# Optimization experiments

Measured on AMD Instinct MI355X. Metric: run time of the kernel, lower is better.

The kernel has to match this reference:

```python
import jax, jax.numpy as jnp
import numpy as np

C_Z = 128
C_H = 128
L = 512
EPS = 1e-5


def _layer_norm(x, w, b):
    mu = jnp.mean(x, axis=-1, keepdims=True)
    var = jnp.mean(jnp.square(x - mu), axis=-1, keepdims=True)
    return (x - mu) * jax.lax.rsqrt(var + EPS) * w + b


def setup_inputs() -> dict:
    key = jax.random.key(0)
    ks = jax.random.split(key, 10)
    s_z = 1.0 / np.sqrt(C_Z)
    s_h = 1.0 / np.sqrt(C_H)
    return {
        "z": jax.random.normal(ks[0], (L, L, C_Z), dtype=jnp.float32),
        "pair_mask": jax.random.randint(ks[1], (L, L), 0, 2, dtype=jnp.int32),
        "ln_in_w": jnp.ones((C_Z,), jnp.float32),
        "ln_in_b": jnp.zeros((C_Z,), jnp.float32),
        "ln_out_w": jnp.ones((C_H,), jnp.float32),
        "ln_out_b": jnp.zeros((C_H,), jnp.float32),
        # weights stored [in, out] so forward is x @ W
        "W_proj_a": jax.random.uniform(ks[2], (C_Z, C_H), jnp.float32, -s_z, s_z),
        "W_gate_a": jax.random.uniform(ks[3], (C_Z, C_H), jnp.float32, -s_z, s_z),
        "W_proj_b": jax.random.uniform(ks[4], (C_Z, C_H), jnp.float32, -s_z, s_z),
        "W_gate_b": jax.random.uniform(ks[5], (C_Z, C_H), jnp.float32, -s_z, s_z),
        "W_gate_out": jax.random.uniform(ks[6], (C_Z, C_Z), jnp.float32, -s_z, s_z),
        "W_proj_out": jax.random.uniform(ks[7], (C_H, C_Z), jnp.float32, -s_h, s_h),
    }


def reference(z, pair_mask, ln_in_w, ln_in_b, ln_out_w, ln_out_b,
              W_proj_a, W_gate_a, W_proj_b, W_gate_b, W_gate_out, W_proj_out):
    mask = pair_mask.astype(z.dtype)[..., None]  # [L, L, 1]
    z_ln = _layer_norm(z, ln_in_w, ln_in_b)      # [L, L, c_z]
    a = jax.nn.sigmoid(z_ln @ W_gate_a) * (z_ln @ W_proj_a) * mask  # [L, L, c_h]
    b = jax.nn.sigmoid(z_ln @ W_gate_b) * (z_ln @ W_proj_b) * mask  # [L, L, c_h]
    m = jnp.einsum('ikc,jkc->ijc', a, b)         # channel-batched matmul
    m_ln = _layer_norm(m, ln_out_w, ln_out_b)
    g = jax.nn.sigmoid(z_ln @ W_gate_out)        # [L, L, c_z]
    dz = g * (m_ln @ W_proj_out)
    return dz * mask
```

## Files before the change

### kernel.cpp

```cpp
#include <hip/hip_runtime.h>
#include <stdint.h>

#define LDIM 512
#define LLTOT 262144
#define EPSV 1e-5f

typedef short bf16x8 __attribute__((ext_vector_type(8)));
typedef float f32x4 __attribute__((ext_vector_type(4)));
typedef __attribute__((address_space(1))) unsigned as1_u32;
typedef __attribute__((address_space(3))) unsigned as3_u32;

__device__ __forceinline__ void stage16(const void* g, void* l) {
  __builtin_amdgcn_global_load_lds((as1_u32*)g, (as3_u32*)l, 16, 0, 0);
}

__device__ __forceinline__ unsigned short f2bf(float f) {
  union { float f; unsigned u; } v; v.f = f;
  unsigned r = v.u + 0x7FFFu + ((v.u >> 16) & 1u);
  return (unsigned short)(r >> 16);
}
__device__ __forceinline__ float bf2f(unsigned short h) {
  union { unsigned u; float f; } v; v.u = ((unsigned)h) << 16;
  return v.f;
}
__device__ __forceinline__ unsigned cvtpk(float lo, float hi) {
  unsigned r;
  asm("v_cvt_pk_bf16_f32 %0, %1, %2" : "=v"(r) : "v"(lo), "v"(hi));
  return r;
}
__device__ __forceinline__ float sigm(float x) { return 1.0f / (1.0f + __expf(-x)); }


__global__ void k_prep(const float* __restrict__ Wpa, const float* __restrict__ Wga,
                       const float* __restrict__ Wpb, const float* __restrict__ Wgb,
                       const float* __restrict__ Wgo, const float* __restrict__ Wpo,
                       unsigned short* __restrict__ Wt) {
  int t = blockIdx.x * blockDim.x + threadIdx.x;
  int mat = t >> 14;
  int rem = t & 16383;
  int o = rem >> 7;
  int c = rem & 127;
  const float* src;
  switch (mat) {
    case 0: src = Wga; break;
    case 1: src = Wpa; break;
    case 2: src = Wgb; break;
    case 3: src = Wpb; break;
    case 4: src = Wgo; break;
    default: src = Wpo; break;
  }
  Wt[mat * 16384 + o * 128 + c] = f2bf(src[c * 128 + o]);
}

__global__ __launch_bounds__(256, 4) void k_proj(const float* __restrict__ z,
                                                 const float* __restrict__ lnw,
                                                 const float* __restrict__ lnb,
                                                 const unsigned short* __restrict__ Wt,
                                                 const int* __restrict__ maskp,
                                                 unsigned short* __restrict__ a_f,
                                                 unsigned short* __restrict__ b_f,
                                                 unsigned short* __restrict__ gout) {
  __shared__ __align__(16) unsigned char zbuf[128 * 272];
  __shared__ float maskf[128];
  const int t = threadIdx.x;
  const int bid = blockIdx.x;
  const long r0 = (long)bid * 128;
  const int w = t >> 6, lane = t & 63;
  const int mn = lane & 15, q4 = lane >> 4;
  const int k0 = (bid & 3) * 128;
  const long ibase = (long)(bid >> 2) * 131072;

  if (t < 128) maskf[t] = (float)maskp[r0 + t];

  {
    const int sub = lane >> 4, c16 = lane & 15;
    const float4 lw0 = ((const float4*)lnw)[c16 * 2];
    const float4 lw1 = ((const float4*)lnw)[c16 * 2 + 1];
    const float4 lb0 = ((const float4*)lnb)[c16 * 2];
    const float4 lb1 = ((const float4*)lnb)[c16 * 2 + 1];
#pragma unroll 2
    for (int rr = 0; rr < 8; ++rr) {
      const int row = w * 32 + rr * 4 + sub;
      const float4* zr = (const float4*)(z + (r0 + row) * 128);
      float4 v0 = zr[c16 * 2], v1 = zr[c16 * 2 + 1];
      float s = ((v0.x + v0.y) + (v0.z + v0.w)) + ((v1.x + v1.y) + (v1.z + v1.w));
      float q = v0.x * v0.x + v0.y * v0.y + v0.z * v0.z + v0.w * v0.w +
                v1.x * v1.x + v1.y * v1.y + v1.z * v1.z + v1.w * v1.w;
#pragma unroll
      for (int off = 8; off; off >>= 1) { s += __shfl_xor(s, off); q += __shfl_xor(q, off); }
      float mu = s * (1.0f / 128.0f);
      float rs = rsqrtf(q * (1.0f / 128.0f) - mu * mu + EPSV);
      uint4 o;
      o.x = cvtpk((v0.x - mu) * rs * lw0.x + lb0.x, (v0.y - mu) * rs * lw0.y + lb0.y);
      o.y = cvtpk((v0.z - mu) * rs * lw0.z + lb0.z, (v0.w - mu) * rs * lw0.w + lb0.w);
      o.z = cvtpk((v1.x - mu) * rs * lw1.x + lb1.x, (v1.y - mu) * rs * lw1.y + lb1.y);
      o.w = cvtpk((v1.z - mu) * rs * lw1.z + lb1.z, (v1.w - mu) * rs * lw1.w + lb1.w);
      *(uint4*)(&zbuf[row * 272 + c16 * 16]) = o;
    }
  }
  __syncthreads();

#pragma unroll 1
  for (int p = 0; p < 2; ++p) {
    const unsigned short* Wg = Wt + (p * 2) * 16384;
    const unsigned short* Wp = Wt + (p * 2 + 1) * 16384;
    unsigned short* dst = p ? b_f : a_f;
    bf16x8 wg[2][4], wp[2][4];
#pragma unroll
    for (int ntl = 0; ntl < 2; ++ntl)
#pragma unroll
      for (int kk = 0; kk < 4; ++kk) {
        const int o = (w * 2 + ntl) * 16 + mn;
        wg[ntl][kk] = *(const bf16x8*)(Wg + o * 128 + kk * 32 + q4 * 8);
        wp[ntl][kk] = *(const bf16x8*)(Wp + o * 128 + kk * 32 + q4 * 8);
      }
#pragma unroll 1
    for (int rg = 0; rg < 8; ++rg) {
      bf16x8 afr[4];
#pragma unroll
      for (int kk = 0; kk < 4; ++kk)
        afr[kk] = *(const bf16x8*)(&zbuf[(rg * 16 + mn) * 272 + kk * 64 + q4 * 16]);
      f32x4 aG[2] = {{0.f,0.f,0.f,0.f},{0.f,0.f,0.f,0.f}};
      f32x4 aP[2] = {{0.f,0.f,0.f,0.f},{0.f,0.f,0.f,0.f}};
#pragma unroll
      for (int kk = 0; kk < 4; ++kk)
#pragma unroll
        for (int ntl = 0; ntl < 2; ++ntl) {
          aG[ntl] = __builtin_amdgcn_mfma_f32_16x16x32_bf16(afr[kk], wg[ntl][kk], aG[ntl], 0, 0, 0);
          aP[ntl] = __builtin_amdgcn_mfma_f32_16x16x32_bf16(afr[kk], wp[ntl][kk], aP[ntl], 0, 0, 0);
        }
      const int rowb = rg * 16 + q4 * 4;
      const int kpos = k0 + rowb;
      char* dst0 = (char*)dst + ibase + (kpos >> 5) * 8192 + (kpos & 31) * 2;
#pragma unroll
      for (int ntl = 0; ntl < 2; ++ntl) {
        const int c = (w * 2 + ntl) * 16 + mn;
        float e0 = sigm(aG[ntl][0]) * aP[ntl][0] * maskf[rowb + 0];
        float e1 = sigm(aG[ntl][1]) * aP[ntl][1] * maskf[rowb + 1];
        float e2 = sigm(aG[ntl][2]) * aP[ntl][2] * maskf[rowb + 2];
        float e3 = sigm(aG[ntl][3]) * aP[ntl][3] * maskf[rowb + 3];
        uint2 pk;
        pk.x = cvtpk(e0, e1);
        pk.y = cvtpk(e2, e3);
        *(uint2*)(dst0 + c * 64) = pk;
      }
    }
  }

  {
    const unsigned short* Wgp = Wt + 4 * 16384;
    bf16x8 wg[2][4];
#pragma unroll
    for (int ntl = 0; ntl < 2; ++ntl)
#pragma unroll
      for (int kk = 0; kk < 4; ++kk)
        wg[ntl][kk] = *(const bf16x8*)(Wgp + ((w * 2 + ntl) * 16 + mn) * 128 + kk * 32 + q4 * 8);
#pragma unroll 1
    for (int rg = 0; rg < 8; ++rg) {
      bf16x8 afr[4];
#pragma unroll
      for (int kk = 0; kk < 4; ++kk)
        afr[kk] = *(const bf16x8*)(&zbuf[(rg * 16 + mn) * 272 + kk * 64 + q4 * 16]);
      f32x4 aG[2] = {{0.f,0.f,0.f,0.f},{0.f,0.f,0.f,0.f}};
#pragma unroll
      for (int kk = 0; kk < 4; ++kk)
#pragma unroll
        for (int ntl = 0; ntl < 2; ++ntl)
          aG[ntl] = __builtin_amdgcn_mfma_f32_16x16x32_bf16(afr[kk], wg[ntl][kk], aG[ntl], 0, 0, 0);
      const int rowb = rg * 16 + q4 * 4;
#pragma unroll
      for (int ntl = 0; ntl < 2; ++ntl) {
        const int c = (w * 2 + ntl) * 16 + mn;
        unsigned u01 = cvtpk(sigm(aG[ntl][0]), sigm(aG[ntl][1]));
        unsigned u23 = cvtpk(sigm(aG[ntl][2]), sigm(aG[ntl][3]));
        gout[(r0 + rowb + 0) * 128 + c] = (unsigned short)u01;
        gout[(r0 + rowb + 1) * 128 + c] = (unsigned short)(u01 >> 16);
        gout[(r0 + rowb + 2) * 128 + c] = (unsigned short)u23;
        gout[(r0 + rowb + 3) * 128 + c] = (unsigned short)(u23 >> 16);
      }
    }
  }
}

__global__ __launch_bounds__(256, 3) void k_einsum(const unsigned short* __restrict__ af_g,
                                                   const unsigned short* __restrict__ bf_g,
                                                   unsigned short* __restrict__ m_t) {
  __shared__ __align__(16) unsigned char shm[49152];
  const int t = threadIdx.x;
  const int w = t >> 6, lane = t & 63;
  const int bid = blockIdx.x;
  const int xcd = bid & 7;
  const int j = bid >> 3;
  const int ch = xcd * 16 + (j >> 4);
  const int tile = j & 15;
  const int ti = tile >> 2, tj = tile & 3;
  const int wr = w >> 1, wc = w & 1;
  const int mn = lane & 15, q4 = lane >> 4;
  const int loff = (mn * 4 + q4) * 16;

  const long lanepart = (long)(lane >> 2) * 131072 + (lane & 3) * 16 + ch * 64;

  const char* gsrc[4];
#pragma unroll
  for (int u = 0; u < 4; ++u) {
    const int f = w * 4 + u;
    gsrc[u] = (f < 8)
        ? (const char*)af_g + (long)(ti * 8 + f) * 16 * 131072 + lanepart
        : (const char*)bf_g + (long)(tj * 8 + (f - 8)) * 16 * 131072 + lanepart;
  }

  f32x4 acc[4][4];
#pragma unroll
  for (int i = 0; i < 4; ++i)
#pragma unroll
    for (int jj = 0; jj < 4; ++jj) acc[i][jj] = (f32x4){0.f, 0.f, 0.f, 0.f};

#define STAGE(q, k32)                                                          \
  {                                                                            \
    _Pragma("unroll")                                                          \
    for (int u = 0; u < 4; ++u)                                                \
      stage16(gsrc[u] + (long)(k32) * 8192,                                    \
              &shm[(q) * 16384 + (w * 4 + u) * 1024]);                         \
  }

  STAGE(0, 0)
  STAGE(1, 1)
#pragma unroll 1
  for (int k32 = 0; k32 < 16; ++k32) {
    if (k32 < 15) {
      asm volatile("s_waitcnt vmcnt(4)\n\ts_barrier" ::: "memory");
    } else {
      asm volatile("s_waitcnt vmcnt(0)\n\ts_barrier" ::: "memory");
    }
    if (k32 + 2 < 16) STAGE((k32 + 2) % 3, k32 + 2)
    const int cb = (k32 % 3) * 16384;
    bf16x8 afr[4], bfr[4];
#pragma unroll
    for (int mt = 0; mt < 4; ++mt)
      afr[mt] = *(const bf16x8*)(&shm[cb + (wr * 4 + mt) * 1024 + loff]);
#pragma unroll
    for (int nt = 0; nt < 4; ++nt)
      bfr[nt] = *(const bf16x8*)(&shm[cb + 8192 + (wc * 4 + nt) * 1024 + loff]);
#pragma unroll
    for (int mt = 0; mt < 4; ++mt)
#pragma unroll
      for (int nt = 0; nt < 4; ++nt)
        acc[mt][nt] = __builtin_amdgcn_mfma_f32_16x16x32_bf16(
            afr[mt], bfr[nt], acc[mt][nt], 0, 0, 0);
  }
#undef STAGE
  __syncthreads();

  unsigned char* eb = shm + w * 9216;
#pragma unroll
  for (int mt = 0; mt < 4; ++mt)
#pragma unroll
    for (int nt = 0; nt < 4; ++nt) {
      const int rlb = mt * 16 + q4 * 4;
      const int cl = nt * 16 + mn;
      unsigned u01 = cvtpk(acc[mt][nt][0], acc[mt][nt][1]);
      unsigned u23 = cvtpk(acc[mt][nt][2], acc[mt][nt][3]);
      *(unsigned short*)(&eb[(rlb + 0) * 144 + cl * 2]) = (unsigned short)u01;
      *(unsigned short*)(&eb[(rlb + 1) * 144 + cl * 2]) = (unsigned short)(u01 >> 16);
      *(unsigned short*)(&eb[(rlb + 2) * 144 + cl * 2]) = (unsigned short)u23;
      *(unsigned short*)(&eb[(rlb + 3) * 144 + cl * 2]) = (unsigned short)(u23 >> 16);
    }
  char* Mg = (char*)m_t + (long)ch * 524288 +
             (long)(ti * 128 + wr * 64) * 1024 + (tj * 128 + wc * 64) * 2;
#pragma unroll
  for (int it = 0; it < 8; ++it) {
    int rl = it * 8 + (lane >> 3), cc = lane & 7;
    *(int4*)(Mg + (long)rl * 1024 + cc * 16) = *(const int4*)(&eb[rl * 144 + cc * 16]);
  }
}

__global__ __launch_bounds__(256, 3) void k_out(const unsigned short* __restrict__ m_t,
                                                const unsigned short* __restrict__ gbuf,
                                                const unsigned short* __restrict__ Wt,
                                                const int* __restrict__ maskp,
                                                const float* __restrict__ lnw,
                                                const float* __restrict__ lnb,
                                                float* __restrict__ out) {
  __shared__ unsigned char mln[64 * 272];
  __shared__ float obuf[64 * 132];
  __shared__ float lw[128], lb[128], mk[64];
  const int t = threadIdx.x;
  const long r0 = (long)blockIdx.x * 64;

#pragma unroll
  for (int it = 0; it < 4; ++it) {
    int chunk = it * 256 + t;
    int c = chunk >> 3, cc = chunk & 7;
    int4 rv = *(const int4*)((const char*)m_t + (long)c * 524288 + r0 * 2 + cc * 16);
    const unsigned short* rp = (const unsigned short*)&rv;
#pragma unroll
    for (int e = 0; e < 8; ++e) {
      int er = (e + cc) & 7;
      *(unsigned short*)(&mln[(cc * 8 + er) * 272 + c * 2]) = rp[er];
    }
  }
  if (t < 128) { lw[t] = lnw[t]; lb[t] = lnb[t]; }
  if (t < 64) mk[t] = (float)maskp[r0 + t];
  __syncthreads();

  {
    int row = t >> 2, part = t & 3;
    float xv[32];
    float s = 0.f, q = 0.f;
#pragma unroll
    for (int jj = 0; jj < 16; ++jj) {
      unsigned u = *(const unsigned*)(&mln[row * 272 + part * 64 + jj * 4]);
      float x0 = bf2f((unsigned short)(u & 0xffff));
      float x1 = bf2f((unsigned short)(u >> 16));
      xv[2 * jj] = x0; xv[2 * jj + 1] = x1;
      s += x0 + x1; q += x0 * x0 + x1 * x1;
    }
    s += __shfl_xor(s, 1); q += __shfl_xor(q, 1);
    s += __shfl_xor(s, 2); q += __shfl_xor(q, 2);
    float mu = s * (1.f / 128.f);
    float var = q * (1.f / 128.f) - mu * mu;
    float rs = rsqrtf(var + EPSV);
#pragma unroll
    for (int jj = 0; jj < 16; ++jj) {
      int c = part * 32 + 2 * jj;
      unsigned pk = cvtpk((xv[2 * jj] - mu) * rs * lw[c] + lb[c],
                          (xv[2 * jj + 1] - mu) * rs * lw[c + 1] + lb[c + 1]);
      *(unsigned*)(&mln[row * 272 + c * 2]) = pk;
    }
  }
  __syncthreads();

  const int w = t >> 6, lane = t & 63;
  const int mn = lane & 15, q4 = lane >> 4;
  bf16x8 afr[4];
#pragma unroll
  for (int kk = 0; kk < 4; ++kk)
    afr[kk] = *(const bf16x8*)(&mln[(w * 16 + mn) * 272 + kk * 64 + q4 * 16]);
  const unsigned short* Wp = Wt + 5 * 16384;
#pragma unroll 1
  for (int nt = 0; nt < 8; ++nt) {
    f32x4 acc = {0.f, 0.f, 0.f, 0.f};
#pragma unroll
    for (int kk = 0; kk < 4; ++kk) {
      bf16x8 bfr = *(const bf16x8*)(Wp + (nt * 16 + mn) * 128 + kk * 32 + q4 * 8);
      acc = __builtin_amdgcn_mfma_f32_16x16x32_bf16(afr[kk], bfr, acc, 0, 0, 0);
    }
    const int cl = nt * 16 + mn;
#pragma unroll
    for (int r = 0; r < 4; ++r)
      obuf[(w * 16 + q4 * 4 + r) * 132 + cl] = acc[r];
  }
  __syncthreads();

#pragma unroll
  for (int it = 0; it < 8; ++it) {
    int chunk = it * 256 + t;
    int row = chunk >> 5, cc = chunk & 31;
    float4 v = *(const float4*)(&obuf[row * 132 + cc * 4]);
    uint2 gp = *(const uint2*)((const char*)gbuf + (r0 + row) * 256 + cc * 8);
    float mval = mk[row];
    v.x *= bf2f((unsigned short)(gp.x & 0xffff)) * mval;
    v.y *= bf2f((unsigned short)(gp.x >> 16)) * mval;
    v.z *= bf2f((unsigned short)(gp.y & 0xffff)) * mval;
    v.w *= bf2f((unsigned short)(gp.y >> 16)) * mval;
    *(float4*)(out + (r0 + row) * 128 + cc * 4) = v;
  }
}

extern "C" void kernel_launch(void* const* d_in, const int* in_sizes, int n_in,
                              void* d_out, int out_size, void* d_ws, size_t ws_size,
                              hipStream_t stream) {
  const float* z    = (const float*)d_in[0];
  const int* maskp  = (const int*)d_in[1];
  const float* lniw = (const float*)d_in[2];
  const float* lnib = (const float*)d_in[3];
  const float* lnow = (const float*)d_in[4];
  const float* lnob = (const float*)d_in[5];
  const float* Wpa  = (const float*)d_in[6];
  const float* Wga  = (const float*)d_in[7];
  const float* Wpb  = (const float*)d_in[8];
  const float* Wgb  = (const float*)d_in[9];
  const float* Wgo  = (const float*)d_in[10];
  const float* Wpo  = (const float*)d_in[11];
  float* out = (float*)d_out;

  char* ws = (char*)d_ws;
  unsigned short* a_f = (unsigned short*)(ws);
  unsigned short* b_f = (unsigned short*)(ws + 67108864);
  unsigned short* g   = (unsigned short*)(ws + 134217728);
  unsigned short* m_t = (unsigned short*)(ws + 201326592);
  unsigned short* Wt  = (unsigned short*)(ws + 268435456);

  k_prep<<<384, 256, 0, stream>>>(Wpa, Wga, Wpb, Wgb, Wgo, Wpo, Wt);
  k_proj<<<2048, 256, 0, stream>>>(z, lniw, lnib, Wt, maskp, a_f, b_f, g);
  k_einsum<<<2048, 256, 0, stream>>>(a_f, b_f, m_t);
  k_out<<<4096, 256, 0, stream>>>(m_t, g, Wt, maskp, lnow, lnob, out);
}
```

Before: 498.9 us.

## Use fast exp2/rcp sigmoid, unroll projection loops, fuse gating into output epilogue

Sigmoid now uses hardware exp2 and reciprocal approximations instead of expf plus a division. The row-group loops in the projection kernel are unrolled by two. In k_out the gate tile is staged into LDS up front and the final gate-times-mask multiply is applied directly in the MFMA epilogue. This removes the fp32 obuf round trip and a barrier, and the occupancy hint is raised to 4 blocks per SM. The trade-off is that output stores become scalar per-lane writes (16 consecutive floats per row group) rather than float4 coalesced rows, and the fast reciprocal is slightly less precise.

Result: faster. 485.3 us (-2.7%).

```diff
diff --git a/kernel.cpp b/kernel.cpp
--- a/kernel.cpp
+++ b/kernel.cpp
@@ -28,7 +28,23 @@
   asm("v_cvt_pk_bf16_f32 %0, %1, %2" : "=v"(r) : "v"(lo), "v"(hi));
   return r;
 }
-__device__ __forceinline__ float sigm(float x) { return 1.0f / (1.0f + __expf(-x)); }
+__device__ __forceinline__ float exp2h(float x) {
+#if __has_builtin(__builtin_amdgcn_exp2f)
+  return __builtin_amdgcn_exp2f(x);
+#else
+  float r; asm("v_exp_f32 %0, %1" : "=v"(r) : "v"(x)); return r;
+#endif
+}
+__device__ __forceinline__ float rcph(float x) {
+#if __has_builtin(__builtin_amdgcn_rcpf)
+  return __builtin_amdgcn_rcpf(x);
+#else
+  float r; asm("v_rcp_f32 %0, %1" : "=v"(r) : "v"(x)); return r;
+#endif
+}
+__device__ __forceinline__ float sigm(float x) {
+  return rcph(1.0f + exp2h(x * -1.44269504f));
+}
 
 
 __global__ void k_prep(const float* __restrict__ Wpa, const float* __restrict__ Wga,
@@ -114,7 +130,7 @@
         wg[ntl][kk] = *(const bf16x8*)(Wg + o * 128 + kk * 32 + q4 * 8);
         wp[ntl][kk] = *(const bf16x8*)(Wp + o * 128 + kk * 32 + q4 * 8);
       }
-#pragma unroll 1
+#pragma unroll 2
     for (int rg = 0; rg < 8; ++rg) {
       bf16x8 afr[4];
 #pragma unroll
@@ -155,7 +171,7 @@
 #pragma unroll
       for (int kk = 0; kk < 4; ++kk)
         wg[ntl][kk] = *(const bf16x8*)(Wgp + ((w * 2 + ntl) * 16 + mn) * 128 + kk * 32 + q4 * 8);
-#pragma unroll 1
+#pragma unroll 2
     for (int rg = 0; rg < 8; ++rg) {
       bf16x8 afr[4];
 #pragma unroll
@@ -274,7 +290,7 @@
   }
 }
 
-__global__ __launch_bounds__(256, 3) void k_out(const unsigned short* __restrict__ m_t,
+__global__ __launch_bounds__(256, 4) void k_out(const unsigned short* __restrict__ m_t,
                                                 const unsigned short* __restrict__ gbuf,
                                                 const unsigned short* __restrict__ Wt,
                                                 const int* __restrict__ maskp,
@@ -282,7 +298,7 @@
                                                 const float* __restrict__ lnb,
                                                 float* __restrict__ out) {
   __shared__ unsigned char mln[64 * 272];
-  __shared__ float obuf[64 * 132];
+  __shared__ unsigned char glds[64 * 272];
   __shared__ float lw[128], lb[128], mk[64];
   const int t = threadIdx.x;
   const long r0 = (long)blockIdx.x * 64;
@@ -298,6 +314,13 @@
       int er = (e + cc) & 7;
       *(unsigned short*)(&mln[(cc * 8 + er) * 272 + c * 2]) = rp[er];
     }
+  }
+#pragma unroll
+  for (int it = 0; it < 4; ++it) {
+    int chunk = it * 256 + t;
+    int row = chunk >> 4, cc = chunk & 15;
+    *(int4*)(&glds[row * 272 + cc * 16]) =
+        *(const int4*)((const char*)gbuf + (r0 + row) * 256 + cc * 16);
   }
   if (t < 128) { lw[t] = lnw[t]; lb[t] = lnb[t]; }
   if (t < 64) mk[t] = (float)maskp[r0 + t];
@@ -347,23 +370,11 @@
     }
     const int cl = nt * 16 + mn;
 #pragma unroll
-    for (int r = 0; r < 4; ++r)
-      obuf[(w * 16 + q4 * 4 + r) * 132 + cl] = acc[r];
-  }
-  __syncthreads();
-
-#pragma unroll
-  for (int it = 0; it < 8; ++it) {
-    int chunk = it * 256 + t;
-    int row = chunk >> 5, cc = chunk & 31;
-    float4 v = *(const float4*)(&obuf[row * 132 + cc * 4]);
-    uint2 gp = *(const uint2*)((const char*)gbuf + (r0 + row) * 256 + cc * 8);
-    float mval = mk[row];
-    v.x *= bf2f((unsigned short)(gp.x & 0xffff)) * mval;
-    v.y *= bf2f((unsigned short)(gp.x >> 16)) * mval;
-    v.z *= bf2f((unsigned short)(gp.y & 0xffff)) * mval;
-    v.w *= bf2f((unsigned short)(gp.y >> 16)) * mval;
-    *(float4*)(out + (r0 + row) * 128 + cc * 4) = v;
+    for (int r = 0; r < 4; ++r) {
+      const int row = w * 16 + q4 * 4 + r;
+      float gv = bf2f(*(const unsigned short*)(&glds[row * 272 + cl * 2]));
+      out[(r0 + row) * 128 + cl] = acc[r] * gv * mk[row];
+    }
   }
 }
 
```
